# Kernel optimization log

Measured on AMD Instinct MI355X. Metric: run time of the kernel, lower is better.

Reference implementation:

```python
import jax, jax.numpy as jnp
import numpy as np

D_MODEL = 1024
D_FF = 4096          # shared expert hidden
NUM_M = 2
E_ROUTER = 8 * NUM_M - 1   # 15 router experts
D_FF_R = D_FF // NUM_M     # 2048 router expert hidden
TOP_K = NUM_M * 2 - 1      # 3
B, T = 2, 2048


def setup_inputs() -> dict:
    key = jax.random.key(0)
    ks = jax.random.split(key, 12)
    s = lambda fan_in: 1.0 / np.sqrt(fan_in)
    x = jax.random.normal(ks[0], (B, T, D_MODEL), dtype=jnp.float32)
    # shared experts stacked [S=1, ...]
    sW1 = jax.random.uniform(ks[1], (1, D_MODEL, D_FF), jnp.float32, -s(D_MODEL), s(D_MODEL))
    sb1 = jax.random.uniform(ks[2], (1, D_FF), jnp.float32, -s(D_MODEL), s(D_MODEL))
    sW2 = jax.random.uniform(ks[3], (1, D_FF, D_MODEL), jnp.float32, -s(D_FF), s(D_FF))
    sb2 = jax.random.uniform(ks[4], (1, D_MODEL), jnp.float32, -s(D_FF), s(D_FF))
    # router experts stacked [E, ...]
    rW1 = jax.random.uniform(ks[5], (E_ROUTER, D_MODEL, D_FF_R), jnp.float32, -s(D_MODEL), s(D_MODEL))
    rb1 = jax.random.uniform(ks[6], (E_ROUTER, D_FF_R), jnp.float32, -s(D_MODEL), s(D_MODEL))
    rW2 = jax.random.uniform(ks[7], (E_ROUTER, D_FF_R, D_MODEL), jnp.float32, -s(D_FF_R), s(D_FF_R))
    rb2 = jax.random.uniform(ks[8], (E_ROUTER, D_MODEL), jnp.float32, -s(D_FF_R), s(D_FF_R))
    # gating linear d_model -> E
    gW = jax.random.uniform(ks[9], (D_MODEL, E_ROUTER), jnp.float32, -s(D_MODEL), s(D_MODEL))
    gb = jax.random.uniform(ks[10], (E_ROUTER,), jnp.float32, -s(D_MODEL), s(D_MODEL))
    return {"x": x, "sW1": sW1, "sb1": sb1, "sW2": sW2, "sb2": sb2,
            "rW1": rW1, "rb1": rb1, "rW2": rW2, "rb2": rb2, "gW": gW, "gb": gb}


def _expert_stack(x, W1, b1, W2, b2):
    # x: [b,t,d]; W1: [e,d,f] -> out [e,b,t,d]
    h = jax.nn.gelu(jnp.einsum('btd,edf->ebtf', x, W1) + b1[:, None, None, :],
                    approximate=False)
    return jnp.einsum('ebtf,efd->ebtd', h, W2) + b2[:, None, None, :]


def reference(x, sW1, sb1, sW2, sb2, rW1, rb1, rW2, rb2, gW, gb):
    # shared experts (sum over S)
    shared_enc = _expert_stack(x, sW1, sb1, sW2, sb2).sum(0)  # [b,t,d]
    # gating: softmax then keep top-k values (no renormalization)
    weights = jax.nn.softmax(x @ gW + gb, axis=-1)            # [b,t,E]
    topv, topi = jax.lax.top_k(weights, TOP_K)                # [b,t,K]
    gated = (jax.nn.one_hot(topi, E_ROUTER, dtype=weights.dtype)
             * topv[..., None]).sum(axis=-2)                  # [b,t,E]
    # dense per-expert compute masked by sparse gates (faithful to source)
    router_out = _expert_stack(x, rW1, rb1, rW2, rb2)         # [E,b,t,d]
    router_enc = jnp.einsum('ebtd,bte->btd', router_out, gated)
    return shared_enc + router_enc + x
```

## Files before the change

kernel.cpp:

```cpp
#include <hip/hip_runtime.h>
#include <hip/hip_bf16.h>
#include <cstdint>
#include <cstddef>

#define TOKENS 4096
#define DM     1024
#define DFF    4096
#define NE     15
#define DFR    2048
#define NEX    17
#define MAXT   176

typedef float f32x4 __attribute__((ext_vector_type(4)));
typedef int   i32x4 __attribute__((ext_vector_type(4)));

__device__ __forceinline__ void mfma_16x16x32_bf16(f32x4& d, i32x4 a, i32x4 b){
  asm("v_mfma_f32_16x16x32_bf16 %0, %1, %2, %0" : "+v"(d) : "v"(a), "v"(b));
}

__device__ __forceinline__ void gload16(const void* g, void* l){
  __builtin_amdgcn_global_load_lds(
      (const __attribute__((address_space(1))) uint32_t*)g,
      (__attribute__((address_space(3))) uint32_t*)l, 16, 0, 0);
}

__device__ __forceinline__ unsigned short f2bf(float f){
  unsigned u = __float_as_uint(f);
  u += 0x7FFFu + ((u >> 16) & 1u);
  return (unsigned short)(u >> 16);
}

__device__ __forceinline__ float gelu_fast(float v){
  float u = 1.5957691216057308f * (v + 0.044715f * v * v * v);
  float e = __expf(-u);
  return v / (1.0f + e);
}


__global__ void tcast_kernel(const float* __restrict__ src, ushort* __restrict__ dst, int R, int C){
  __shared__ float tile[32][33];
  const size_t bo = (size_t)blockIdx.z * R * C;
  const int c0 = blockIdx.x*32, r0 = blockIdx.y*32;
  const int tx = threadIdx.x, ty = threadIdx.y;
  #pragma unroll
  for (int i=0;i<4;i++){
    int r = ty + i*8;
    tile[r][tx] = src[bo + (size_t)(r0+r)*C + c0 + tx];
  }
  __syncthreads();
  #pragma unroll
  for (int i=0;i<4;i++){
    int r = ty + i*8;
    dst[bo + (size_t)(c0+r)*R + r0 + tx] = f2bf(tile[tx][r]);
  }
}


__global__ void gate_kernel(const float* __restrict__ x, const float* __restrict__ gW,
                            const float* __restrict__ gb, ushort* __restrict__ xb,
                            int* __restrict__ tokexp, float* __restrict__ tokp){
  const int wave = threadIdx.x >> 6, lane = threadIdx.x & 63;
  const int token = blockIdx.x*4 + wave;
  const float* xr = x + (size_t)token * DM;
  float a[NE];
  #pragma unroll
  for (int e=0;e<NE;e++) a[e] = 0.f;
  const int d0 = lane * 16;
  float xv[16];
  #pragma unroll
  for (int j=0;j<4;j++){
    float4 v = reinterpret_cast<const float4*>(xr + d0)[j];
    xv[j*4+0]=v.x; xv[j*4+1]=v.y; xv[j*4+2]=v.z; xv[j*4+3]=v.w;
  }
  {
    ushort o[16];
    #pragma unroll
    for (int j=0;j<16;j++) o[j] = f2bf(xv[j]);
    ushort* dst = xb + (size_t)token*DM + d0;
    *reinterpret_cast<i32x4*>(dst)     = *reinterpret_cast<const i32x4*>(&o[0]);
    *reinterpret_cast<i32x4*>(dst + 8) = *reinterpret_cast<const i32x4*>(&o[8]);
  }
  for (int j=0;j<16;j++){
    const float* gr = gW + (size_t)(d0 + j) * NE;
    #pragma unroll
    for (int e=0;e<NE;e++) a[e] += xv[j]*gr[e];
  }
  #pragma unroll
  for (int e=0;e<NE;e++){
    for (int off=32; off; off>>=1) a[e] += __shfl_xor(a[e], off, 64);
  }
  if (lane == 0){
    float l[NE], p[NE];
    float m = -1e30f;
    for (int e=0;e<NE;e++){ l[e] = a[e] + gb[e]; m = fmaxf(m, l[e]); }
    float s = 0.f;
    for (int e=0;e<NE;e++){ p[e] = expf(l[e]-m); s += p[e]; }
    float inv = 1.f/s;
    unsigned used = 0;
    for (int k=0;k<3;k++){
      int best = -1; float bv = -1e30f;
      for (int e=0;e<NE;e++) if (!((used>>e)&1u) && l[e] > bv){ bv = l[e]; best = e; }
      used |= 1u<<best;
      tokexp[token*3 + k] = best;
      tokp[token*3 + k]   = p[best]*inv;
    }
  }
}


__global__ void assign_kernel(const int* __restrict__ tokexp, const float* __restrict__ tokp,
                              int* __restrict__ counts, int* __restrict__ bases,
                              int* __restrict__ tokidx, float* __restrict__ gatev,
                              int* __restrict__ tokslot,
                              int* __restrict__ tile_e, int* __restrict__ tile_by,
                              int* __restrict__ ntiles){
  __shared__ int lh[256][NE];
  const int tid = threadIdx.x;
  const int t0 = tid * 16;

  int le[48];
  #pragma unroll
  for (int e=0;e<NE;e++) lh[tid][e] = 0;
  #pragma unroll
  for (int j=0;j<48;j++){
    int e = tokexp[t0*3 + j];
    le[j] = e;
    lh[tid][e]++;
  }
  __syncthreads();
  if (tid < NE){
    int run = 0;
    for (int i=0;i<256;i++){
      int v = lh[i][tid];
      lh[i][tid] = run;
      run += v;
    }
    counts[tid] = run;
  }
  __syncthreads();
  if (tid == 0){
    int b = 0, t = 0;
    for (int e=0;e<NE;e++){
      int c = counts[e];
      int prows = ((c+127)>>7)<<7;
      bases[e] = b; b += prows;
      int nb = prows >> 7;
      for (int j=0;j<nb && t<MAXT;j++){ tile_e[t]=e; tile_by[t]=j; t++; }
    }
    bases[NE] = b; bases[NE+1] = b + TOKENS;
    for (int e=NE;e<NEX;e++){
      for (int j=0;j<32 && t<MAXT;j++){ tile_e[t]=e; tile_by[t]=j; t++; }
    }
    ntiles[0] = t;
  }
  __syncthreads();
  #pragma unroll
  for (int j=0;j<48;j++){
    const int t = t0 + (j/3), k = j - (j/3)*3;
    const int e = le[j];
    const int slot = lh[tid][e]++;
    const int idx = e*TOKENS + slot;
    tokidx[idx] = t;
    gatev[idx]  = tokp[t*3 + k];
    tokslot[t*3 + k] = idx;
  }
}


__global__ __launch_bounds__(256,3) void gemm1_kernel(
    const ushort* __restrict__ xb, const ushort* __restrict__ rW1T,
    const ushort* __restrict__ sW1T, const float* __restrict__ rb1,
    const float* __restrict__ sb1, const int* __restrict__ counts,
    const int* __restrict__ bases, const int* __restrict__ tokidx,
    const int* __restrict__ tile_e, const int* __restrict__ tile_by,
    const int* __restrict__ ntiles, ushort* __restrict__ h)
{
  const int ty = blockIdx.y;
  if (ty >= ntiles[0]) return;
  const int e = tile_e[ty], by = tile_by[ty], bx = blockIdx.x;
  const int cnt = (e < NE) ? counts[e] : TOKENS;

  __shared__ __align__(16) ushort lA[128*64];
  __shared__ __align__(16) ushort lB[128*64];

  const int tid = threadIdx.x, wave = tid >> 6, lane = tid & 63;
  const int wr = wave >> 1, wc = wave & 1;

  const ushort* Bp = (e < NE) ? (rW1T + ((size_t)e*DFR + (size_t)bx*128)*DM)
                              : (sW1T + ((size_t)(e-NE)*DFR + (size_t)bx*128)*DM);

  const ushort* srcA[4];
  const ushort* srcB[4];
  unsigned ldso[4];
  #pragma unroll
  for (int i=0;i<4;i++){
    const int rt = i*32 + wave*8 + (lane>>3);
    const int gr = by*128 + rt;
    const int tok = (e < NE) ? tokidx[e*TOKENS + (gr < cnt ? gr : cnt-1)] : gr;
    srcA[i] = xb + (size_t)tok*DM + (lane&7)*8;
    srcB[i] = Bp + (size_t)rt*DM + (lane&7)*8;
    ldso[i] = (unsigned)(i*4096 + wave*1024 + lane*16);
  }

  f32x4 acc[4][4];
  #pragma unroll
  for (int m=0;m<4;m++){
    #pragma unroll
    for (int n=0;n<4;n++){ acc[m][n] = (f32x4){0.f,0.f,0.f,0.f}; }
  }

  for (int k0=0; k0<DM; k0+=64){
    __syncthreads();
    #pragma unroll
    for (int i=0;i<4;i++){ gload16(srcA[i]+k0, (char*)lA + ldso[i]); }
    #pragma unroll
    for (int i=0;i<4;i++){ gload16(srcB[i]+k0, (char*)lB + ldso[i]); }
    __syncthreads();
    #pragma unroll
    for (int kk=0; kk<2; kk++){
      i32x4 af[4], bfr[4];
      #pragma unroll
      for (int m=0;m<4;m++){
        af[m] = *(const i32x4*)((const char*)lA + ((wr*64 + m*16 + (lane&15))*128 + kk*64 + (lane>>4)*16));
      }
      #pragma unroll
      for (int n=0;n<4;n++){
        bfr[n] = *(const i32x4*)((const char*)lB + ((wc*64 + n*16 + (lane&15))*128 + kk*64 + (lane>>4)*16));
      }
      #pragma unroll
      for (int m=0;m<4;m++){
        #pragma unroll
        for (int n=0;n<4;n++){ mfma_16x16x32_bf16(acc[m][n], af[m], bfr[n]); }
      }
    }
  }

  const int hb = bases[e];
  const float* b1p = (e < NE) ? (rb1 + e*DFR + bx*128) : (sb1 + (e-NE)*DFR + bx*128);
  #pragma unroll
  for (int m=0;m<4;m++){
    #pragma unroll
    for (int n=0;n<4;n++){
      const int c = wc*64 + n*16 + (lane & 15);
      const float bias = b1p[c];
      #pragma unroll
      for (int i=0;i<4;i++){
        const int r = wr*64 + m*16 + (lane>>4)*4 + i;
        float v = acc[m][n][i] + bias;
        h[(size_t)(hb + by*128 + r)*DFR + (size_t)bx*128 + c] = f2bf(gelu_fast(v));
      }
    }
  }
}


__global__ __launch_bounds__(256,3) void gemm2_kernel(
    const ushort* __restrict__ hbuf, const ushort* __restrict__ rW2T,
    const ushort* __restrict__ sW2T, const float* __restrict__ rb2,
    const float* __restrict__ sb2, const int* __restrict__ counts,
    const int* __restrict__ bases,
    const int* __restrict__ tile_e, const int* __restrict__ tile_by,
    const int* __restrict__ ntiles, ushort* __restrict__ rout)
{
  const int ty = blockIdx.y;
  if (ty >= ntiles[0]) return;
  const int e = tile_e[ty], by = tile_by[ty], bx = blockIdx.x;

  __shared__ __align__(16) ushort lA[128*64];
  __shared__ __align__(16) ushort lB[128*64];

  const int tid = threadIdx.x, wave = tid >> 6, lane = tid & 63;
  const int wr = wave >> 1, wc = wave & 1;

  const int hb = bases[e];
  const ushort* Ab = hbuf + (size_t)(hb + by*128)*DFR;
  const ushort* Bp; size_t ldb;
  if (e < NE){ Bp = rW2T + ((size_t)e*DM + (size_t)bx*128)*DFR; ldb = DFR; }
  else       { Bp = sW2T + (size_t)(bx*128)*DFF + (size_t)(e-NE)*DFR; ldb = DFF; }

  const ushort* srcA[4];
  const ushort* srcB[4];
  unsigned ldso[4];
  #pragma unroll
  for (int i=0;i<4;i++){
    const int rt = i*32 + wave*8 + (lane>>3);
    srcA[i] = Ab + (size_t)rt*DFR + (lane&7)*8;
    srcB[i] = Bp + (size_t)rt*ldb + (lane&7)*8;
    ldso[i] = (unsigned)(i*4096 + wave*1024 + lane*16);
  }

  f32x4 acc[4][4];
  #pragma unroll
  for (int m=0;m<4;m++){
    #pragma unroll
    for (int n=0;n<4;n++){ acc[m][n] = (f32x4){0.f,0.f,0.f,0.f}; }
  }

  for (int k0=0; k0<DFR; k0+=64){
    __syncthreads();
    #pragma unroll
    for (int i=0;i<4;i++){ gload16(srcA[i]+k0, (char*)lA + ldso[i]); }
    #pragma unroll
    for (int i=0;i<4;i++){ gload16(srcB[i]+k0, (char*)lB + ldso[i]); }
    __syncthreads();
    #pragma unroll
    for (int kk=0; kk<2; kk++){
      i32x4 af[4], bfr[4];
      #pragma unroll
      for (int m=0;m<4;m++){
        af[m] = *(const i32x4*)((const char*)lA + ((wr*64 + m*16 + (lane&15))*128 + kk*64 + (lane>>4)*16));
      }
      #pragma unroll
      for (int n=0;n<4;n++){
        bfr[n] = *(const i32x4*)((const char*)lB + ((wc*64 + n*16 + (lane&15))*128 + kk*64 + (lane>>4)*16));
      }
      #pragma unroll
      for (int m=0;m<4;m++){
        #pragma unroll
        for (int n=0;n<4;n++){ mfma_16x16x32_bf16(acc[m][n], af[m], bfr[n]); }
      }
    }
  }

  #pragma unroll
  for (int m=0;m<4;m++){
    #pragma unroll
    for (int n=0;n<4;n++){
      const int c  = wc*64 + n*16 + (lane & 15);
      const int cg = bx*128 + c;
      const float bias = (e < NE) ? rb2[e*DM + cg] : ((e == NE) ? sb2[cg] : 0.f);
      #pragma unroll
      for (int i=0;i<4;i++){
        const int r = wr*64 + m*16 + (lane>>4)*4 + i;
        rout[(size_t)(hb + by*128 + r)*DM + cg] = f2bf(acc[m][n][i] + bias);
      }
    }
  }
}


__global__ void combine_kernel(const float* __restrict__ x, const ushort* __restrict__ rout,
                               const int* __restrict__ bases, const int* __restrict__ tokslot,
                               const float* __restrict__ gatev, float* __restrict__ out)
{
  const int wave = threadIdx.x >> 6, lane = threadIdx.x & 63;
  const int token = blockIdx.x*4 + wave;
  const int d0 = lane*16;

  float acc[16];
  #pragma unroll
  for (int j=0;j<4;j++){
    float4 v = reinterpret_cast<const float4*>(x + (size_t)token*DM + d0)[j];
    acc[j*4+0]=v.x; acc[j*4+1]=v.y; acc[j*4+2]=v.z; acc[j*4+3]=v.w;
  }

  int   rows[5];
  float gs[5];
  rows[0] = bases[NE]   + token; gs[0] = 1.f;
  rows[1] = bases[NE+1] + token; gs[1] = 1.f;
  #pragma unroll
  for (int k=0;k<3;k++){
    const int idx = tokslot[token*3 + k];
    const int e = idx >> 12, s = idx & (TOKENS-1);
    rows[2+k] = bases[e] + s;
    gs[2+k] = gatev[idx];
  }

  #pragma unroll
  for (int q=0;q<5;q++){
    const float g = gs[q];
    const ushort* rp = rout + (size_t)rows[q]*DM + d0;
    #pragma unroll
    for (int hh=0;hh<2;hh++){
      i32x4 v = *reinterpret_cast<const i32x4*>(rp + hh*8);
      #pragma unroll
      for (int j=0;j<4;j++){
        const unsigned u = (unsigned)v[j];
        acc[hh*8 + j*2 + 0] += g * __uint_as_float(u << 16);
        acc[hh*8 + j*2 + 1] += g * __uint_as_float(u & 0xFFFF0000u);
      }
    }
  }

  #pragma unroll
  for (int j=0;j<4;j++){
    float4 v; v.x=acc[j*4+0]; v.y=acc[j*4+1]; v.z=acc[j*4+2]; v.w=acc[j*4+3];
    reinterpret_cast<float4*>(out + (size_t)token*DM + d0)[j] = v;
  }
}


extern "C" void kernel_launch(void* const* d_in, const int* in_sizes, int n_in,
                              void* d_out, int out_size, void* d_ws, size_t ws_size,
                              hipStream_t stream)
{
  (void)in_sizes; (void)n_in; (void)out_size; (void)ws_size;
  const float* x   = (const float*)d_in[0];
  const float* sW1 = (const float*)d_in[1];
  const float* sb1 = (const float*)d_in[2];
  const float* sW2 = (const float*)d_in[3];
  const float* sb2 = (const float*)d_in[4];
  const float* rW1 = (const float*)d_in[5];
  const float* rb1 = (const float*)d_in[6];
  const float* rW2 = (const float*)d_in[7];
  const float* rb2 = (const float*)d_in[8];
  const float* gW  = (const float*)d_in[9];
  const float* gb  = (const float*)d_in[10];
  float* out = (float*)d_out;

  char* ws = (char*)d_ws;
  ushort* xb   = (ushort*)(ws + 0);
  ushort* sW1T = (ushort*)(ws + 8388608);
  ushort* sW2T = (ushort*)(ws + 16777216);
  ushort* rW1T = (ushort*)(ws + 25165824);
  ushort* rW2T = (ushort*)(ws + 88080384);
  ushort* hbuf = (ushort*)(ws + 150994944);
  ushort* rout = (ushort*)(ws + 25165824);
  int*   counts  = (int*)(ws + 243269632);
  int*   bases   = (int*)(ws + 243269760);
  int*   tokidx  = (int*)(ws + 243270144);
  float* gatev   = (float*)(ws + 243515904);
  int*   tokslot = (int*)(ws + 243761664);
  int*   tokexp  = (int*)(ws + 243810816);
  float* tokp    = (float*)(ws + 243859968);
  int*   tile_e  = (int*)(ws + 243909120);
  int*   tile_by = (int*)(ws + 243910144);
  int*   ntiles  = (int*)(ws + 243911168);

  tcast_kernel<<<dim3(DFF/32, DM/32, 1),  dim3(32,8), 0, stream>>>(sW1, sW1T, DM, DFF);
  tcast_kernel<<<dim3(DM/32, DFF/32, 1),  dim3(32,8), 0, stream>>>(sW2, sW2T, DFF, DM);
  tcast_kernel<<<dim3(DFR/32, DM/32, NE), dim3(32,8), 0, stream>>>(rW1, rW1T, DM, DFR);
  tcast_kernel<<<dim3(DM/32, DFR/32, NE), dim3(32,8), 0, stream>>>(rW2, rW2T, DFR, DM);

  gate_kernel<<<dim3(TOKENS/4), dim3(256), 0, stream>>>(x, gW, gb, xb, tokexp, tokp);
  assign_kernel<<<dim3(1), dim3(256), 0, stream>>>(tokexp, tokp, counts, bases,
                                                   tokidx, gatev, tokslot,
                                                   tile_e, tile_by, ntiles);

  gemm1_kernel<<<dim3(16,MAXT), dim3(256), 0, stream>>>(
      xb, rW1T, sW1T, rb1, sb1, counts, bases, tokidx, tile_e, tile_by, ntiles, hbuf);
  gemm2_kernel<<<dim3(8,MAXT), dim3(256), 0, stream>>>(
      hbuf, rW2T, sW2T, rb2, sb2, counts, bases, tile_e, tile_by, ntiles, rout);
  combine_kernel<<<dim3(TOKENS/4), dim3(256), 0, stream>>>(
      x, rout, bases, tokslot, gatev, out);
}
```

Before: 409.1 us.

## Use 256x256 GEMM tiles with double-buffered swizzled LDS and ping-pong MFMA scheduling

Both expert GEMMs move from 128x128 tiles with 256 threads to 256x256 tiles with 512 threads, a 128 KB double-buffered LDS stage with XOR-swizzled addressing, and interleaved LDS-load/MFMA phases separated by barriers and setprio. The tile list is rebuilt for 256-row tiles, and stores are guarded against padded rows. The aim is more data reuse per loaded tile, fewer LDS bank conflicts, and global loads overlapped with MFMA. In exchange, padding waste grows on small expert groups, fewer blocks run per CU, and register pressure rises from the 8x4 accumulator array.

Result: slower. 444.5 us (+8.6%).

```diff
diff --git a/kernel.cpp b/kernel.cpp
--- a/kernel.cpp
+++ b/kernel.cpp
@@ -9,7 +9,7 @@
 #define NE     15
 #define DFR    2048
 #define NEX    17
-#define MAXT   176
+#define MAXT   104
 
 typedef float f32x4 __attribute__((ext_vector_type(4)));
 typedef int   i32x4 __attribute__((ext_vector_type(4)));
@@ -144,12 +144,12 @@
       int c = counts[e];
       int prows = ((c+127)>>7)<<7;
       bases[e] = b; b += prows;
-      int nb = prows >> 7;
+      int nb = (prows + 255) >> 8;
       for (int j=0;j<nb && t<MAXT;j++){ tile_e[t]=e; tile_by[t]=j; t++; }
     }
     bases[NE] = b; bases[NE+1] = b + TOKENS;
     for (int e=NE;e<NEX;e++){
-      for (int j=0;j<32 && t<MAXT;j++){ tile_e[t]=e; tile_by[t]=j; t++; }
+      for (int j=0;j<16 && t<MAXT;j++){ tile_e[t]=e; tile_by[t]=j; t++; }
     }
     ntiles[0] = t;
   }
@@ -167,7 +167,71 @@
 }
 
 
-__global__ __launch_bounds__(256,3) void gemm1_kernel(
+#define MFMA_PHASE(Q)                                                 \
+  __builtin_amdgcn_s_setprio(1);                                      \
+  _Pragma("unroll")                                                   \
+  for (int k=0;k<2;k++){                                              \
+    _Pragma("unroll")                                                 \
+    for (int mm=0;mm<2;mm++){                                         \
+      _Pragma("unroll")                                               \
+      for (int n=0;n<4;n++){                                          \
+        mfma_16x16x32_bf16(acc[(Q)*2+mm][n], af[mm][k], bf[n][k]);    \
+      } } }                                                           \
+  __builtin_amdgcn_s_setprio(0);
+
+#define LOAD_A(Q)                                                     \
+  _Pragma("unroll")                                                   \
+  for (int mm=0;mm<2;mm++){                                           \
+    const int row_ = wr*128 + ((Q)*2+mm)*16 + (lane&15);              \
+    af[mm][0] = *(const i32x4*)(bp + row_*128 + cb0);                 \
+    af[mm][1] = *(const i32x4*)(bp + row_*128 + cb1);                 \
+  }
+
+#define STAGE_TILE(BUF, T)                                            \
+  { char* dA_ = smem + (size_t)(BUF)*65536;                           \
+    char* dB_ = dA_ + 32768;                                          \
+    _Pragma("unroll")                                                 \
+    for (int s=0;s<4;s++){                                            \
+      gload16(srcA[s] + (size_t)(T)*128, dA_ + sdo[s]);               \
+      gload16(srcB[s] + (size_t)(T)*128, dB_ + sdo[s]);               \
+    } }
+
+#define GEMM_KLOOP(NK)                                                \
+  STAGE_TILE(0, 0);                                                   \
+  asm volatile("s_waitcnt vmcnt(0)" ::: "memory");                    \
+  __builtin_amdgcn_s_barrier();                                       \
+  for (int t=0; t<(NK); ++t){                                         \
+    const char* bp = smem + (size_t)(t&1)*65536;                      \
+    const char* bq = bp + 32768;                                      \
+    i32x4 af[2][2], bf[4][2];                                         \
+    _Pragma("unroll")                                                 \
+    for (int n=0;n<4;n++){                                            \
+      const int row_ = wc*64 + n*16 + (lane&15);                      \
+      bf[n][0] = *(const i32x4*)(bq + row_*128 + cb0);                \
+      bf[n][1] = *(const i32x4*)(bq + row_*128 + cb1);                \
+    }                                                                 \
+    LOAD_A(0);                                                        \
+    if (t+1 < (NK)){ STAGE_TILE((t+1)&1, t+1); }                      \
+    __builtin_amdgcn_s_barrier();                                     \
+    MFMA_PHASE(0);                                                    \
+    __builtin_amdgcn_s_barrier();                                     \
+    LOAD_A(1);                                                        \
+    __builtin_amdgcn_s_barrier();                                     \
+    MFMA_PHASE(1);                                                    \
+    __builtin_amdgcn_s_barrier();                                     \
+    LOAD_A(2);                                                        \
+    __builtin_amdgcn_s_barrier();                                     \
+    MFMA_PHASE(2);                                                    \
+    __builtin_amdgcn_s_barrier();                                     \
+    LOAD_A(3);                                                        \
+    __builtin_amdgcn_s_barrier();                                     \
+    MFMA_PHASE(3);                                                    \
+    if (t+1 < (NK)) asm volatile("s_waitcnt vmcnt(0)" ::: "memory");  \
+    __builtin_amdgcn_s_barrier();                                     \
+  }
+
+
+__global__ __launch_bounds__(512,2) void gemm1_kernel(
     const ushort* __restrict__ xb, const ushort* __restrict__ rW1T,
     const ushort* __restrict__ sW1T, const float* __restrict__ rb1,
     const float* __restrict__ sb1, const int* __restrict__ counts,
@@ -179,82 +243,64 @@
   if (ty >= ntiles[0]) return;
   const int e = tile_e[ty], by = tile_by[ty], bx = blockIdx.x;
   const int cnt = (e < NE) ? counts[e] : TOKENS;
-
-  __shared__ __align__(16) ushort lA[128*64];
-  __shared__ __align__(16) ushort lB[128*64];
-
+  const int prows = (e < NE) ? (((cnt+127)>>7)<<7) : TOKENS;
+
+  __shared__ __align__(16) char smem[131072];
   const int tid = threadIdx.x, wave = tid >> 6, lane = tid & 63;
-  const int wr = wave >> 1, wc = wave & 1;
-
-  const ushort* Bp = (e < NE) ? (rW1T + ((size_t)e*DFR + (size_t)bx*128)*DM)
-                              : (sW1T + ((size_t)(e-NE)*DFR + (size_t)bx*128)*DM);
-
-  const ushort* srcA[4];
-  const ushort* srcB[4];
-  unsigned ldso[4];
-  #pragma unroll
-  for (int i=0;i<4;i++){
-    const int rt = i*32 + wave*8 + (lane>>3);
-    const int gr = by*128 + rt;
-    const int tok = (e < NE) ? tokidx[e*TOKENS + (gr < cnt ? gr : cnt-1)] : gr;
-    srcA[i] = xb + (size_t)tok*DM + (lane&7)*8;
-    srcB[i] = Bp + (size_t)rt*DM + (lane&7)*8;
-    ldso[i] = (unsigned)(i*4096 + wave*1024 + lane*16);
-  }
-
-  f32x4 acc[4][4];
-  #pragma unroll
-  for (int m=0;m<4;m++){
+  const int wr = wave >> 2, wc = wave & 3;
+
+  const unsigned swc = (unsigned)((((lane&7) ^ (lane>>3)) & 7) << 4);
+  const unsigned cb0 = (unsigned)((((lane>>4)<<4)) ^ ((lane&7)<<4));
+  const unsigned cb1 = cb0 ^ 64u;
+
+  const char* Bpb = (e < NE) ? (const char*)rW1T + (size_t)e*DFR*2048
+                             : (const char*)sW1T + (size_t)(e-NE)*DFR*2048;
+  const char* srcA[4];
+  const char* srcB[4];
+  unsigned sdo[4];
+  #pragma unroll
+  for (int s=0;s<4;s++){
+    const int row = (wave*4+s)*8 + (lane>>3);
+    const int gr = by*256 + row;
+    int tok;
+    if (e < NE){ const int cr = gr < cnt ? gr : cnt-1; tok = tokidx[e*TOKENS + cr]; }
+    else       { tok = gr; }
+    srcA[s] = (const char*)xb + (size_t)tok*2048 + swc;
+    srcB[s] = Bpb + (size_t)(bx*256 + row)*2048 + swc;
+    sdo[s]  = (unsigned)((wave*4+s)*1024 + lane*16);
+  }
+
+  f32x4 acc[8][4];
+  #pragma unroll
+  for (int m=0;m<8;m++){
     #pragma unroll
     for (int n=0;n<4;n++){ acc[m][n] = (f32x4){0.f,0.f,0.f,0.f}; }
   }
 
-  for (int k0=0; k0<DM; k0+=64){
-    __syncthreads();
-    #pragma unroll
-    for (int i=0;i<4;i++){ gload16(srcA[i]+k0, (char*)lA + ldso[i]); }
-    #pragma unroll
-    for (int i=0;i<4;i++){ gload16(srcB[i]+k0, (char*)lB + ldso[i]); }
-    __syncthreads();
-    #pragma unroll
-    for (int kk=0; kk<2; kk++){
-      i32x4 af[4], bfr[4];
-      #pragma unroll
-      for (int m=0;m<4;m++){
-        af[m] = *(const i32x4*)((const char*)lA + ((wr*64 + m*16 + (lane&15))*128 + kk*64 + (lane>>4)*16));
+  GEMM_KLOOP(DM/64)
+
+  const int hb = bases[e];
+  const float* b1p = (e < NE) ? (rb1 + e*DFR + bx*256) : (sb1 + (e-NE)*DFR + bx*256);
+  #pragma unroll
+  for (int m=0;m<8;m++){
+    const int rt = wr*128 + m*16 + (lane>>4)*4;
+    #pragma unroll
+    for (int i=0;i<4;i++){
+      const int gr = by*256 + rt + i;
+      if (gr < prows){
+        #pragma unroll
+        for (int n=0;n<4;n++){
+          const int c = wc*64 + n*16 + (lane & 15);
+          float v = acc[m][n][i] + b1p[c];
+          h[(size_t)(hb + gr)*DFR + (size_t)bx*256 + c] = f2bf(gelu_fast(v));
+        }
       }
-      #pragma unroll
-      for (int n=0;n<4;n++){
-        bfr[n] = *(const i32x4*)((const char*)lB + ((wc*64 + n*16 + (lane&15))*128 + kk*64 + (lane>>4)*16));
-      }
-      #pragma unroll
-      for (int m=0;m<4;m++){
-        #pragma unroll
-        for (int n=0;n<4;n++){ mfma_16x16x32_bf16(acc[m][n], af[m], bfr[n]); }
-      }
-    }
-  }
-
-  const int hb = bases[e];
-  const float* b1p = (e < NE) ? (rb1 + e*DFR + bx*128) : (sb1 + (e-NE)*DFR + bx*128);
-  #pragma unroll
-  for (int m=0;m<4;m++){
-    #pragma unroll
-    for (int n=0;n<4;n++){
-      const int c = wc*64 + n*16 + (lane & 15);
-      const float bias = b1p[c];
-      #pragma unroll
-      for (int i=0;i<4;i++){
-        const int r = wr*64 + m*16 + (lane>>4)*4 + i;
-        float v = acc[m][n][i] + bias;
-        h[(size_t)(hb + by*128 + r)*DFR + (size_t)bx*128 + c] = f2bf(gelu_fast(v));
-      }
-    }
-  }
-}
-
-
-__global__ __launch_bounds__(256,3) void gemm2_kernel(
+    }
+  }
+}
+
+
+__global__ __launch_bounds__(512,2) void gemm2_kernel(
     const ushort* __restrict__ hbuf, const ushort* __restrict__ rW2T,
     const ushort* __restrict__ sW2T, const float* __restrict__ rb2,
     const float* __restrict__ sb2, const int* __restrict__ counts,
@@ -265,74 +311,57 @@
   const int ty = blockIdx.y;
   if (ty >= ntiles[0]) return;
   const int e = tile_e[ty], by = tile_by[ty], bx = blockIdx.x;
-
-  __shared__ __align__(16) ushort lA[128*64];
-  __shared__ __align__(16) ushort lB[128*64];
-
+  const int cnt = (e < NE) ? counts[e] : TOKENS;
+  const int prows = (e < NE) ? (((cnt+127)>>7)<<7) : TOKENS;
+  const int hb = bases[e];
+
+  __shared__ __align__(16) char smem[131072];
   const int tid = threadIdx.x, wave = tid >> 6, lane = tid & 63;
-  const int wr = wave >> 1, wc = wave & 1;
-
-  const int hb = bases[e];
-  const ushort* Ab = hbuf + (size_t)(hb + by*128)*DFR;
-  const ushort* Bp; size_t ldb;
-  if (e < NE){ Bp = rW2T + ((size_t)e*DM + (size_t)bx*128)*DFR; ldb = DFR; }
-  else       { Bp = sW2T + (size_t)(bx*128)*DFF + (size_t)(e-NE)*DFR; ldb = DFF; }
-
-  const ushort* srcA[4];
-  const ushort* srcB[4];
-  unsigned ldso[4];
-  #pragma unroll
-  for (int i=0;i<4;i++){
-    const int rt = i*32 + wave*8 + (lane>>3);
-    srcA[i] = Ab + (size_t)rt*DFR + (lane&7)*8;
-    srcB[i] = Bp + (size_t)rt*ldb + (lane&7)*8;
-    ldso[i] = (unsigned)(i*4096 + wave*1024 + lane*16);
-  }
-
-  f32x4 acc[4][4];
-  #pragma unroll
-  for (int m=0;m<4;m++){
+  const int wr = wave >> 2, wc = wave & 3;
+
+  const unsigned swc = (unsigned)((((lane&7) ^ (lane>>3)) & 7) << 4);
+  const unsigned cb0 = (unsigned)((((lane>>4)<<4)) ^ ((lane&7)<<4));
+  const unsigned cb1 = cb0 ^ 64u;
+
+  const char* srcA[4];
+  const char* srcB[4];
+  unsigned sdo[4];
+  #pragma unroll
+  for (int s=0;s<4;s++){
+    const int row = (wave*4+s)*8 + (lane>>3);
+    int ar = by*256 + row; if (ar >= prows) ar = prows-1;
+    srcA[s] = (const char*)hbuf + (size_t)(hb + ar)*4096 + swc;
+    if (e < NE){
+      srcB[s] = (const char*)rW2T + ((size_t)e*DM + bx*256 + row)*4096 + swc;
+    } else {
+      srcB[s] = (const char*)sW2T + (size_t)(bx*256 + row)*8192 + (size_t)(e-NE)*4096 + swc;
+    }
+    sdo[s]  = (unsigned)((wave*4+s)*1024 + lane*16);
+  }
+
+  f32x4 acc[8][4];
+  #pragma unroll
+  for (int m=0;m<8;m++){
     #pragma unroll
     for (int n=0;n<4;n++){ acc[m][n] = (f32x4){0.f,0.f,0.f,0.f}; }
   }
 
-  for (int k0=0; k0<DFR; k0+=64){
-    __syncthreads();
-    #pragma unroll
-    for (int i=0;i<4;i++){ gload16(srcA[i]+k0, (char*)lA + ldso[i]); }
-    #pragma unroll
-    for (int i=0;i<4;i++){ gload16(srcB[i]+k0, (char*)lB + ldso[i]); }
-    __syncthreads();
-    #pragma unroll
-    for (int kk=0; kk<2; kk++){
-      i32x4 af[4], bfr[4];
-      #pragma unroll
-      for (int m=0;m<4;m++){
-        af[m] = *(const i32x4*)((const char*)lA + ((wr*64 + m*16 + (lane&15))*128 + kk*64 + (lane>>4)*16));
-      }
-      #pragma unroll
-      for (int n=0;n<4;n++){
-        bfr[n] = *(const i32x4*)((const char*)lB + ((wc*64 + n*16 + (lane&15))*128 + kk*64 + (lane>>4)*16));
-      }
-      #pragma unroll
-      for (int m=0;m<4;m++){
+  GEMM_KLOOP(DFR/64)
+
+  #pragma unroll
+  for (int m=0;m<8;m++){
+    const int rt = wr*128 + m*16 + (lane>>4)*4;
+    #pragma unroll
+    for (int i=0;i<4;i++){
+      const int gr = by*256 + rt + i;
+      if (gr < prows){
         #pragma unroll
-        for (int n=0;n<4;n++){ mfma_16x16x32_bf16(acc[m][n], af[m], bfr[n]); }
-      }
-    }
-  }
-
-  #pragma unroll
-  for (int m=0;m<4;m++){
-    #pragma unroll
-    for (int n=0;n<4;n++){
-      const int c  = wc*64 + n*16 + (lane & 15);
-      const int cg = bx*128 + c;
-      const float bias = (e < NE) ? rb2[e*DM + cg] : ((e == NE) ? sb2[cg] : 0.f);
-      #pragma unroll
-      for (int i=0;i<4;i++){
-        const int r = wr*64 + m*16 + (lane>>4)*4 + i;
-        rout[(size_t)(hb + by*128 + r)*DM + cg] = f2bf(acc[m][n][i] + bias);
+        for (int n=0;n<4;n++){
+          const int c  = wc*64 + n*16 + (lane & 15);
+          const int cg = bx*256 + c;
+          const float bias = (e < NE) ? rb2[e*DM + cg] : ((e == NE) ? sb2[cg] : 0.f);
+          rout[(size_t)(hb + gr)*DM + cg] = f2bf(acc[m][n][i] + bias);
+        }
       }
     }
   }
@@ -437,9 +466,9 @@
                                                    tokidx, gatev, tokslot,
                                                    tile_e, tile_by, ntiles);
 
-  gemm1_kernel<<<dim3(16,MAXT), dim3(256), 0, stream>>>(
+  gemm1_kernel<<<dim3(8,MAXT), dim3(512), 0, stream>>>(
       xb, rW1T, sW1T, rb1, sb1, counts, bases, tokidx, tile_e, tile_by, ntiles, hbuf);
-  gemm2_kernel<<<dim3(8,MAXT), dim3(256), 0, stream>>>(
+  gemm2_kernel<<<dim3(4,MAXT), dim3(512), 0, stream>>>(
       hbuf, rW2T, sW2T, rb2, sb2, counts, bases, tile_e, tile_by, ntiles, rout);
   combine_kernel<<<dim3(TOKENS/4), dim3(256), 0, stream>>>(
       x, rout, bases, tokslot, gatev, out);
```
